# Optimization experiments

Measured on AMD Instinct MI355X. Metric: run time of the kernel, lower is better.

## Reference

```python
import jax, jax.numpy as jnp
import numpy as np

N, L, V = 8192, 50, 50000   # sentences, max words/sentence, vocab
D, H, O = 300, 150, 64      # embed dim, SAGE hidden, SAGE out
THRESH = 0.7
NEG = -1e9


def _sage_pool(h, A, mask, W1s, W1n, b1, W2s, W2n, b2, gw, gb):
    """Two-layer mean-aggregator SAGEConv + GlobalAttentionPooling, vectorized
    over N independent per-sentence graphs.
    h:[N,L,din] node feats, A:[N,L,L] bool adjacency (src u -> dst v), mask:[N,L] valid nodes."""
    Af = A.astype(h.dtype)
    deg = jnp.maximum(Af.sum(axis=1), 1.0)  # in-degree per dst node [N,L]

    def conv(x, Ws, Wn, b):
        m = jnp.einsum('nuv,nud->nvd', Af, x) / deg[..., None]  # mean of in-neighbors
        return x @ Ws + m @ Wn + b  # fc_self(x) + fc_neigh(mean)

    h1 = jax.nn.relu(conv(h, W1s, W1n, b1))
    h2 = conv(h1, W2s, W2n, b2)
    # global attention pooling: softmax(gate) over real nodes of each graph
    gate = jnp.squeeze(h2 @ gw, -1) + gb  # [N,L]
    attn = jax.nn.softmax(jnp.where(mask, gate, NEG), axis=-1)
    return jnp.einsum('nl,nld->nd', attn, h2)  # [N,O]


def setup_inputs() -> dict:
    key = jax.random.key(0)
    ks = jax.random.split(key, 32)
    pos = jnp.arange(L)
    lengths = jax.random.randint(ks[0], (N,), 5, L + 1)
    valid = pos[None, :] < lengths[:, None]  # [N,L] real-word mask (0 = pad)
    words = jax.random.randint(ks[1], (N, L), 1, V) * valid
    syntax_words = jax.random.randint(ks[2], (N, L), 1, V) * valid
    adj = jax.random.uniform(ks[3], (N, L, L)) < 0.08
    syntax_adj = (adj & valid[:, :, None] & valid[:, None, :]).astype(jnp.int32)
    hsg_feature = jax.random.normal(ks[4], (N, O), jnp.float32)

    def lin(k, i, o):
        return jax.random.normal(k, (i, o), jnp.float32) / np.sqrt(i)

    inp = {
        'words': words.astype(jnp.int32),
        'syntax_words': syntax_words.astype(jnp.int32),
        'syntax_adj': syntax_adj,
        'hsg_feature': hsg_feature,
        'embed': jax.random.normal(ks[5], (V, D), jnp.float32) * 0.1,
        'sem_W1s': lin(ks[6], D, H), 'sem_W1n': lin(ks[7], D, H), 'sem_b1': jnp.zeros((H,), jnp.float32),
        'sem_W2s': lin(ks[8], H, O), 'sem_W2n': lin(ks[9], H, O), 'sem_b2': jnp.zeros((O,), jnp.float32),
        'sem_gw': lin(ks[10], O, 1), 'sem_gb': jnp.zeros((1,), jnp.float32),
        'syn_W1s': lin(ks[11], D, H), 'syn_W1n': lin(ks[12], D, H), 'syn_b1': jnp.zeros((H,), jnp.float32),
        'syn_W2s': lin(ks[13], H, O), 'syn_W2n': lin(ks[14], H, O), 'syn_b2': jnp.zeros((O,), jnp.float32),
        'syn_gw': lin(ks[15], O, 1), 'syn_gb': jnp.zeros((1,), jnp.float32),
        'cls_w1': lin(ks[16], 3 * O, 128), 'cls_b1': jnp.zeros((128,), jnp.float32),
        'cls_w2': lin(ks[17], 128, 2), 'cls_b2': jnp.zeros((2,), jnp.float32),
    }
    return inp


def reference(words, syntax_words, syntax_adj, hsg_feature, embed,
              sem_W1s, sem_W1n, sem_b1, sem_W2s, sem_W2n, sem_b2, sem_gw, sem_gb,
              syn_W1s, syn_W1n, syn_b1, syn_W2s, syn_W2n, syn_b2, syn_gw, syn_gb,
              cls_w1, cls_b1, cls_w2, cls_b2):
    # --- semantic graph: per-sentence cosine-similarity thresholding ---
    mask = words > 0
    emb = embed[words]  # [N,L,D] gather
    nrm = emb / jnp.maximum(jnp.linalg.norm(emb, axis=-1, keepdims=True), 1e-8)
    cos = jnp.einsum('nld,nmd->nlm', nrm, nrm)  # [N,L,L]
    semA = (cos > THRESH) & mask[:, :, None] & mask[:, None, :]  # includes self-loops (cos=1)
    sem_feat = _sage_pool(emb, semA, mask,
                          sem_W1s, sem_W1n, sem_b1, sem_W2s, sem_W2n, sem_b2, sem_gw, sem_gb)
    # --- syntax graph: given per-sentence adjacency over its word ids ---
    syn_mask = syntax_words > 0
    syn_emb = embed[syntax_words]
    syn_feat = _sage_pool(syn_emb, syntax_adj.astype(bool), syn_mask,
                          syn_W1s, syn_W1n, syn_b1, syn_W2s, syn_W2n, syn_b2, syn_gw, syn_gb)
    # --- concat with HSG sentence state, classify ---
    feat = jnp.concatenate([sem_feat, syn_feat, hsg_feature], axis=-1)  # [N,192]
    hid = jax.nn.relu(feat @ cls_w1 + cls_b1)
    return hid @ cls_w2 + cls_b2  # [N,2]
```

## Files before the change

### kernel.cpp

```cpp
#include <hip/hip_runtime.h>

#define NS 8192
#define L  50

typedef unsigned short u16;
typedef unsigned int   u32;
typedef __attribute__((ext_vector_type(8))) __bf16 bf16x8;
typedef __attribute__((ext_vector_type(4))) float  f32x4;

#define OFF_X    0
#define OFF_TT   0
#define OFF_T2T  0
#define OFF_ATTN 0
#define OFF_H1   21760
#define OFF_RED  21760
#define OFF_M    43264
#define OFF_DIAG 43264
#define OFF_WID  52480
#define OFF_CLO  52736
#define OFF_CHI  52992
#define OFF_RDEG 53248
#define SMEM_SZ  53504

#define XSTR  328
#define TSTR  68
#define H1STR 168
#define MSTR  72

#define W1_ROWS 320
#define W1_KP   328
#define W2_ROWS 128
#define W2_KP   168

__device__ __forceinline__ u16 f2bf(float f) {
  u32 u = __float_as_uint(f);
  u += 0x7fffu + ((u >> 16) & 1u);
  return (u16)(u >> 16);
}
__device__ __forceinline__ float bf2f(u16 h) {
  return __uint_as_float(((u32)h) << 16);
}
__device__ __forceinline__ f32x4 mfma16(bf16x8 a, bf16x8 b, f32x4 c) {
  return __builtin_amdgcn_mfma_f32_16x16x32_bf16(a, b, c, 0, 0, 0);
}
__device__ __forceinline__ uint2 pack4bf(f32x4 c) {
  uint2 p;
  p.x = (u32)f2bf(c[0]) | ((u32)f2bf(c[1]) << 16);
  p.y = (u32)f2bf(c[2]) | ((u32)f2bf(c[3]) << 16);
  return p;
}
union BF8U { bf16x8 v; uint4 u; };
__device__ __forceinline__ bf16x8 ld_bf8_b64pair(const u16* p) {
  uint2 a = *(const uint2*)p;
  uint2 b = *(const uint2*)(p + 4);
  BF8U r; r.u = make_uint4(a.x, a.y, b.x, b.y);
  return r.v;
}

struct GParams {
  const int* words; const int* syn_words; const int* syn_adj;
  const float* embed;
  const float* sem_b1; const float* sem_b2; const float* sem_gw; const float* sem_gb;
  const float* syn_b1; const float* syn_b2; const float* syn_gw; const float* syn_gb;
  const u16* w1t_sem; const u16* w1t_syn; const u16* w2t_sem; const u16* w2t_syn;
  float* semf; float* synf;
};

__global__ __launch_bounds__(256, 3) void sage_kernel(GParams P) {
  __shared__ __align__(16) char smem[SMEM_SZ];
  int*   wid   = (int*)(smem + OFF_WID);
  u32*   clo   = (u32*)(smem + OFF_CLO);
  u32*   chi   = (u32*)(smem + OFF_CHI);
  float* rdegp = (float*)(smem + OFF_RDEG);
  float* diag  = (float*)(smem + OFF_DIAG);

  const int tid  = threadIdx.x;
  const int lane = tid & 63;
  const int w    = tid >> 6;
  const int ln   = lane & 15;
  const int quad = lane >> 4;

  const bool semg = (blockIdx.x < NS);
  const int  n    = semg ? blockIdx.x : (blockIdx.x - NS);

  const int*   wsrc = semg ? P.words   : P.syn_words;
  const u16*   W1T  = semg ? P.w1t_sem : P.w1t_syn;
  const u16*   W2T  = semg ? P.w2t_sem : P.w2t_syn;
  const float* b1g  = semg ? P.sem_b1  : P.syn_b1;
  const float* b2g  = semg ? P.sem_b2  : P.syn_b2;
  const float* gw   = semg ? P.sem_gw  : P.syn_gw;
  const float* gb   = semg ? P.sem_gb  : P.syn_gb;
  float* featout    = semg ? P.semf    : P.synf;

  const int jts[3] = {w, w + 4, 8 + (w & 1)};

  if (tid < 64) {
    wid[tid] = (tid < L) ? wsrc[(size_t)n * L + tid] : 0;
    clo[tid] = 0u; chi[tid] = 0u;
  }
  __syncthreads();

  for (int i = 0; i < 16; ++i) {
    const int v = w + 4 * i;
    const int word = wid[v];
    const float* src = P.embed + (size_t)word * 300;
    u16* xrow = (u16*)(smem + OFF_X) + v * XSTR;
    for (int l = lane; l < 82; l += 64) {
      uint2 pk = make_uint2(0u, 0u);
      if (word > 0 && l < 75) {
        float4 f = *(const float4*)(src + l * 4);
        pk.x = (u32)f2bf(f.x) | ((u32)f2bf(f.y) << 16);
        pk.y = (u32)f2bf(f.z) | ((u32)f2bf(f.w) << 16);
      }
      *(uint2*)(xrow + l * 4) = pk;
    }
  }
  __syncthreads();

  if (semg) {
    const f32x4 z4 = {0.f, 0.f, 0.f, 0.f};
    f32x4 g[4] = {z4, z4, z4, z4};
    const char* xb = smem + OFF_X;
    const int arow = (w * 16 + ln) * (XSTR * 2) + quad * 16;
    for (int kk = 0; kk < 10; ++kk) {
      bf16x8 a = *(const bf16x8*)(xb + arow + kk * 64);
      #pragma unroll
      for (int nt = 0; nt < 4; ++nt) {
        bf16x8 b = *(const bf16x8*)(xb + (nt * 16 + ln) * (XSTR * 2) + quad * 16 + kk * 64);
        g[nt] = mfma16(a, b, g[nt]);
      }
    }
    {
      const int r = ln - quad * 4;
      if (r >= 0 && r < 4) {
        #pragma unroll
        for (int nt = 0; nt < 4; ++nt) {
          if (nt == w) {
            float val = (r == 0) ? g[nt][0] : (r == 1) ? g[nt][1]
                      : (r == 2) ? g[nt][2] : g[nt][3];
            diag[w * 16 + ln] = val;
          }
        }
      }
    }
    __syncthreads();
    if (tid < 64) { float dd = diag[tid]; diag[tid] = 1.0f / sqrtf(fmaxf(dd, 1e-12f)); }
    __syncthreads();
    {
      const int ubase = w * 16 + quad * 4;
      float ru[4]; int uok[4];
      #pragma unroll
      for (int r = 0; r < 4; ++r) { ru[r] = diag[ubase + r]; uok[r] = wid[ubase + r] > 0; }
      #pragma unroll
      for (int nt = 0; nt < 4; ++nt) {
        const int v = nt * 16 + ln;
        const float rv = diag[v];
        const bool vok = wid[v] > 0;
        u32 nib = 0u;
        #pragma unroll
        for (int r = 0; r < 4; ++r) {
          float c = g[nt][r] * ru[r] * rv;
          if (vok && uok[r] && c > 0.7f) nib |= (1u << r);
        }
        if (nib) {
          if (ubase < 32) atomicOr(&clo[v], nib << ubase);
          else            atomicOr(&chi[v], nib << (ubase - 32));
        }
      }
    }
  } else {
    const int* abase = P.syn_adj + (size_t)n * (L * L);
    for (int v = w; v < L; v += 4) {
      int val = (lane < L) ? abase[lane * L + v] : 0;
      unsigned long long m = __ballot(val != 0);
      if (lane == 0) { clo[v] = (u32)m; chi[v] = (u32)(m >> 32); }
    }
  }
  __syncthreads();

  if (tid < 64) {
    int dg = __popc(clo[tid]) + __popc(chi[tid]);
    rdegp[tid] = 1.0f / (float)(dg > 0 ? dg : 1);
  }
  {
    const int v = lane, half = w;
    const u32 src = (half < 2) ? clo[v] : chi[v];
    const int sh = (half & 1) * 16;
    u16* Mrow = (u16*)(smem + OFF_M) + v * MSTR + half * 16;
    #pragma unroll
    for (int c = 0; c < 4; ++c) {
      uint2 pk;
      u32 b0 = (src >> (sh + 4 * c + 0)) & 1u;
      u32 b1 = (src >> (sh + 4 * c + 1)) & 1u;
      u32 b2 = (src >> (sh + 4 * c + 2)) & 1u;
      u32 b3 = (src >> (sh + 4 * c + 3)) & 1u;
      pk.x = (b0 ? 0x3F80u : 0u) | (b1 ? 0x3F800000u : 0u);
      pk.y = (b2 ? 0x3F80u : 0u) | (b3 ? 0x3F800000u : 0u);
      *(uint2*)(Mrow + 4 * c) = pk;
    }
  }

  const f32x4 z4 = {0.f, 0.f, 0.f, 0.f};
  f32x4 tacc[3][4], sacc[3][4];
  #pragma unroll
  for (int i = 0; i < 3; ++i)
    #pragma unroll
    for (int m = 0; m < 4; ++m) { tacc[i][m] = z4; sacc[i][m] = z4; }
  {
    const char* xb = smem + OFF_X;
    for (int kk = 0; kk < 10; ++kk) {
      bf16x8 x[4];
      #pragma unroll
      for (int m = 0; m < 4; ++m)
        x[m] = *(const bf16x8*)(xb + (m * 16 + ln) * (XSTR * 2) + quad * 16 + kk * 64);
      bf16x8 bn[3], as[3];
      #pragma unroll
      for (int i = 0; i < 3; ++i) {
        const int jt = jts[i];
        bn[i] = *(const bf16x8*)(W1T + (size_t)(jt * 16 + ln) * W1_KP + kk * 32 + quad * 8);
        as[i] = *(const bf16x8*)(W1T + (size_t)((jt + 10) * 16 + ln) * W1_KP + kk * 32 + quad * 8);
      }
      #pragma unroll
      for (int i = 0; i < 3; ++i)
        #pragma unroll
        for (int m = 0; m < 4; ++m) {
          tacc[i][m] = mfma16(x[m], bn[i], tacc[i][m]);
          sacc[i][m] = mfma16(as[i], x[m], sacc[i][m]);
        }
    }
  }
  __syncthreads();

  {
    u16* tt = (u16*)(smem + OFF_TT);
    #pragma unroll
    for (int i = 0; i < 3; ++i) {
      const int jt = jts[i];
      #pragma unroll
      for (int m = 0; m < 4; ++m) {
        const int v0 = m * 16 + quad * 4;
        *(uint2*)(tt + (jt * 16 + ln) * TSTR + v0) = pack4bf(tacc[i][m]);
      }
    }
  }

  bf16x8 mb0[4], mb1[4];
  {
    const u16* Mp = (const u16*)(smem + OFF_M);
    #pragma unroll
    for (int vt = 0; vt < 4; ++vt) {
      mb0[vt] = *(const bf16x8*)(Mp + (vt * 16 + ln) * MSTR + quad * 8);
      mb1[vt] = *(const bf16x8*)(Mp + (vt * 16 + ln) * MSTR + quad * 8 + 32);
    }
  }
  float rd[4];
  #pragma unroll
  for (int vt = 0; vt < 4; ++vt) rd[vt] = rdegp[vt * 16 + ln];
  {
    const u16* tt = (const u16*)(smem + OFF_TT);
    u16* h1p = (u16*)(smem + OFF_H1);
    #pragma unroll
    for (int i = 0; i < 3; ++i) {
      const int jt = jts[i];
      f32x4 gacc[4] = {z4, z4, z4, z4};
      const u16* tb = tt + (jt * 16 + ln) * TSTR + quad * 8;
      bf16x8 ta0 = ld_bf8_b64pair(tb);
      bf16x8 ta1 = ld_bf8_b64pair(tb + 32);
      #pragma unroll
      for (int vt = 0; vt < 4; ++vt) {
        gacc[vt] = mfma16(ta0, mb0[vt], gacc[vt]);
        gacc[vt] = mfma16(ta1, mb1[vt], gacc[vt]);
      }
      const int j0 = jt * 16 + quad * 4;
      float bv[4];
      #pragma unroll
      for (int r = 0; r < 4; ++r) { int j = j0 + r; bv[r] = (j < 150) ? b1g[j] : 0.f; }
      #pragma unroll
      for (int vt = 0; vt < 4; ++vt) {
        const int v = vt * 16 + ln;
        f32x4 hv;
        #pragma unroll
        for (int r = 0; r < 4; ++r)
          hv[r] = fmaxf(sacc[i][vt][r] + gacc[vt][r] * rd[vt] + bv[r], 0.f);
        *(uint2*)(h1p + v * H1STR + j0) = pack4bf(hv);
      }
    }
  }
  __syncthreads();

  f32x4 s2acc[4] = {z4, z4, z4, z4};
  f32x4 h2v[4];
  {
    f32x4 t2acc[4] = {z4, z4, z4, z4};
    const u16* h1p = (const u16*)(smem + OFF_H1);
    for (int kk = 0; kk < 5; ++kk) {
      bf16x8 h[4];
      #pragma unroll
      for (int t4 = 0; t4 < 4; ++t4)
        h[t4] = *(const bf16x8*)(h1p + (t4 * 16 + ln) * H1STR + kk * 32 + quad * 8);
      bf16x8 a2  = *(const bf16x8*)(W2T + (size_t)(w * 16 + ln) * W2_KP + kk * 32 + quad * 8);
      bf16x8 b2f = *(const bf16x8*)(W2T + (size_t)((4 + w) * 16 + ln) * W2_KP + kk * 32 + quad * 8);
      #pragma unroll
      for (int vt = 0; vt < 4; ++vt) {
        s2acc[vt] = mfma16(a2, h[vt], s2acc[vt]);
        t2acc[vt] = mfma16(h[vt], b2f, t2acc[vt]);
      }
    }
    u16* t2t = (u16*)(smem + OFF_T2T);
    #pragma unroll
    for (int m = 0; m < 4; ++m) {
      const int v0 = m * 16 + quad * 4;
      *(uint2*)(t2t + (w * 16 + ln) * TSTR + v0) = pack4bf(t2acc[m]);
    }
    f32x4 g2[4] = {z4, z4, z4, z4};
    const u16* t2b = t2t + (w * 16 + ln) * TSTR + quad * 8;
    bf16x8 u0 = ld_bf8_b64pair(t2b);
    bf16x8 u1 = ld_bf8_b64pair(t2b + 32);
    #pragma unroll
    for (int vt = 0; vt < 4; ++vt) {
      g2[vt] = mfma16(u0, mb0[vt], g2[vt]);
      g2[vt] = mfma16(u1, mb1[vt], g2[vt]);
    }
    const int j0q = w * 16 + quad * 4;
    float b2v[4];
    #pragma unroll
    for (int r = 0; r < 4; ++r) b2v[r] = b2g[j0q + r];
    #pragma unroll
    for (int vt = 0; vt < 4; ++vt)
      #pragma unroll
      for (int r = 0; r < 4; ++r)
        h2v[vt][r] = s2acc[vt][r] + g2[vt][r] * rd[vt] + b2v[r];
  }
  __syncthreads();

  {
    const int j0q = w * 16 + quad * 4;
    float gwv[4];
    #pragma unroll
    for (int r = 0; r < 4; ++r) gwv[r] = gw[j0q + r];
    float* redp = (float*)(smem + OFF_RED);
    #pragma unroll
    for (int vt = 0; vt < 4; ++vt) {
      float p = h2v[vt][0] * gwv[0] + h2v[vt][1] * gwv[1]
              + h2v[vt][2] * gwv[2] + h2v[vt][3] * gwv[3];
      redp[(vt * 16 + ln) * 17 + (w * 4 + quad)] = p;
    }
  }
  __syncthreads();

  if (tid < 64) {
    const float* redp = (const float*)(smem + OFF_RED);
    float g = gb[0];
    #pragma unroll
    for (int i = 0; i < 16; ++i) g += redp[tid * 17 + i];
    const bool val = wid[tid] > 0;
    g = val ? g : -1e30f;
    float mx = g;
    #pragma unroll
    for (int off = 32; off; off >>= 1) mx = fmaxf(mx, __shfl_xor(mx, off));
    float e = val ? __expf(g - mx) : 0.f;
    float ssum = e;
    #pragma unroll
    for (int off = 32; off; off >>= 1) ssum += __shfl_xor(ssum, off);
    ((float*)(smem + OFF_ATTN))[tid] = e / ssum;
  }
  __syncthreads();

  {
    const float* attnp = (const float*)(smem + OFF_ATTN);
    float av[4];
    #pragma unroll
    for (int vt = 0; vt < 4; ++vt) av[vt] = attnp[vt * 16 + ln];
    float xr[4];
    #pragma unroll
    for (int r = 0; r < 4; ++r) {
      float x = av[0] * h2v[0][r] + av[1] * h2v[1][r]
              + av[2] * h2v[2][r] + av[3] * h2v[3][r];
      #pragma unroll
      for (int off = 1; off < 16; off <<= 1) x += __shfl_xor(x, off);
      xr[r] = x;
    }
    if (ln == 0) {
      const int j0q = w * 16 + quad * 4;
      *(float4*)(featout + (size_t)n * 64 + j0q) = make_float4(xr[0], xr[1], xr[2], xr[3]);
    }
  }
}

__global__ void prep_w1(const float* Wn, const float* Ws, u16* dst) {
  int idx = blockIdx.x * 256 + threadIdx.x;
  if (idx >= W1_ROWS * W1_KP) return;
  int nn = idx / W1_KP, k = idx - nn * W1_KP;
  float v = 0.f;
  if (k < 300) {
    if (nn < 150) v = Wn[k * 150 + nn];
    else if (nn >= 160 && nn < 310) v = Ws[k * 150 + (nn - 160)];
  }
  dst[idx] = f2bf(v);
}
__global__ void prep_w2(const float* Ws, const float* Wn, u16* dst) {
  int idx = blockIdx.x * 256 + threadIdx.x;
  if (idx >= W2_ROWS * W2_KP) return;
  int nn = idx / W2_KP, k = idx - nn * W2_KP;
  float v = 0.f;
  if (k < 150) v = (nn < 64) ? Ws[k * 64 + nn] : Wn[k * 64 + (nn - 64)];
  dst[idx] = f2bf(v);
}

__global__ __launch_bounds__(128) void cls_kernel(const float* semf, const float* synf,
                                                  const float* hsg,
                                                  const float* w1, const float* b1,
                                                  const float* w2, const float* b2,
                                                  float* out) {
  __shared__ float feat[32][192];
  __shared__ float hid[32][132];
  const int r0 = blockIdx.x * 32;
  for (int idx = threadIdx.x; idx < 32 * 192; idx += 128) {
    int r = idx / 192, c = idx % 192;
    float v;
    if (c < 64)        v = semf[(size_t)(r0 + r) * 64 + c];
    else if (c < 128)  v = synf[(size_t)(r0 + r) * 64 + (c - 64)];
    else               v = hsg [(size_t)(r0 + r) * 64 + (c - 128)];
    feat[r][c] = v;
  }
  __syncthreads();
  {
    const int j = threadIdx.x;
    float acc[32];
    float bb = b1[j];
    #pragma unroll
    for (int r = 0; r < 32; ++r) acc[r] = bb;
    for (int k = 0; k < 192; ++k) {
      float ww = w1[(size_t)k * 128 + j];
      #pragma unroll
      for (int r = 0; r < 32; ++r) acc[r] += feat[r][k] * ww;
    }
    #pragma unroll
    for (int r = 0; r < 32; ++r) hid[r][j] = fmaxf(acc[r], 0.0f);
  }
  __syncthreads();
  if (threadIdx.x < 64) {
    const int r = threadIdx.x >> 1, o = threadIdx.x & 1;
    float a = b2[o];
    for (int h = 0; h < 128; ++h) a += hid[r][h] * w2[h * 2 + o];
    out[(size_t)(r0 + r) * 2 + o] = a;
  }
}

extern "C" void kernel_launch(void* const* d_in, const int* in_sizes, int n_in,
                              void* d_out, int out_size, void* d_ws, size_t ws_size,
                              hipStream_t stream) {
  GParams P;
  P.words     = (const int*)d_in[0];
  P.syn_words = (const int*)d_in[1];
  P.syn_adj   = (const int*)d_in[2];
  const float* hsg = (const float*)d_in[3];
  P.embed   = (const float*)d_in[4];
  const float* sem_W1s = (const float*)d_in[5];
  const float* sem_W1n = (const float*)d_in[6];
  P.sem_b1  = (const float*)d_in[7];
  const float* sem_W2s = (const float*)d_in[8];
  const float* sem_W2n = (const float*)d_in[9];
  P.sem_b2  = (const float*)d_in[10];
  P.sem_gw  = (const float*)d_in[11];
  P.sem_gb  = (const float*)d_in[12];
  const float* syn_W1s = (const float*)d_in[13];
  const float* syn_W1n = (const float*)d_in[14];
  P.syn_b1  = (const float*)d_in[15];
  const float* syn_W2s = (const float*)d_in[16];
  const float* syn_W2n = (const float*)d_in[17];
  P.syn_b2  = (const float*)d_in[18];
  P.syn_gw  = (const float*)d_in[19];
  P.syn_gb  = (const float*)d_in[20];
  const float* cls_w1 = (const float*)d_in[21];
  const float* cls_b1 = (const float*)d_in[22];
  const float* cls_w2 = (const float*)d_in[23];
  const float* cls_b2 = (const float*)d_in[24];

  float* semf = (float*)d_ws;
  float* synf = semf + (size_t)NS * 64;
  u16* w1t_sem = (u16*)((char*)d_ws + (size_t)4 * 1024 * 1024);
  u16* w1t_syn = w1t_sem + W1_ROWS * W1_KP;
  u16* w2t_sem = w1t_syn + W1_ROWS * W1_KP;
  u16* w2t_syn = w2t_sem + W2_ROWS * W2_KP;
  P.semf = semf; P.synf = synf;
  P.w1t_sem = w1t_sem; P.w1t_syn = w1t_syn;
  P.w2t_sem = w2t_sem; P.w2t_syn = w2t_syn;

  const int g1 = (W1_ROWS * W1_KP + 255) / 256;
  const int g2 = (W2_ROWS * W2_KP + 255) / 256;
  prep_w1<<<g1, 256, 0, stream>>>(sem_W1n, sem_W1s, w1t_sem);
  prep_w1<<<g1, 256, 0, stream>>>(syn_W1n, syn_W1s, w1t_syn);
  prep_w2<<<g2, 256, 0, stream>>>(sem_W2s, sem_W2n, w2t_sem);
  prep_w2<<<g2, 256, 0, stream>>>(syn_W2s, syn_W2n, w2t_syn);

  sage_kernel<<<2 * NS, 256, 0, stream>>>(P);
  cls_kernel<<<NS / 32, 128, 0, stream>>>(semf, synf, hsg, cls_w1, cls_b1,
                                          cls_w2, cls_b2, (float*)d_out);
}
```

Baseline: 882.9 us.

## Split layer-1 SAGE GEMM by role across warps and drop persistent adjacency fragments

Layer 1 is re-partitioned by role. Warps 0-1 compute the neighbour-transform tiles (5 each), which they write to LDS. Warps 2-3 compute the self-transform tiles and then do the adjacency aggregation and ReLU, replacing the earlier scheme where every warp did both for 3 tiles and tiles 8-9 were duplicated. Adjacency fragments are now reloaded from LDS at each use instead of being held in registers for the whole kernel, and accumulator count drops, to cut register pressure and redundant MFMA work. Embedding bf16 conversion becomes a cheaper round-half-up, and the LDS layout is repacked with a narrower M stride, at the cost of an extra barrier, load imbalance during aggregation, and possibly misaligned 16-byte LDS reads.

```diff
diff --git a/kernel.cpp b/kernel.cpp
--- a/kernel.cpp
+++ b/kernel.cpp
@@ -11,21 +11,21 @@
 #define OFF_X    0
 #define OFF_TT   0
 #define OFF_T2T  0
-#define OFF_ATTN 0
+#define OFF_RED  8704
+#define OFF_ATTN 13056
 #define OFF_H1   21760
-#define OFF_RED  21760
 #define OFF_M    43264
 #define OFF_DIAG 43264
-#define OFF_WID  52480
-#define OFF_CLO  52736
-#define OFF_CHI  52992
-#define OFF_RDEG 53248
-#define SMEM_SZ  53504
+#define OFF_WID  51968
+#define OFF_CLO  52224
+#define OFF_CHI  52480
+#define OFF_RDEG 52736
+#define SMEM_SZ  52992
 
 #define XSTR  328
 #define TSTR  68
 #define H1STR 168
-#define MSTR  72
+#define MSTR  68
 
 #define W1_ROWS 320
 #define W1_KP   328
@@ -36,9 +36,6 @@
   u32 u = __float_as_uint(f);
   u += 0x7fffu + ((u >> 16) & 1u);
   return (u16)(u >> 16);
-}
-__device__ __forceinline__ float bf2f(u16 h) {
-  return __uint_as_float(((u32)h) << 16);
 }
 __device__ __forceinline__ f32x4 mfma16(bf16x8 a, bf16x8 b, f32x4 c) {
   return __builtin_amdgcn_mfma_f32_16x16x32_bf16(a, b, c, 0, 0, 0);
@@ -91,8 +88,6 @@
   const float* gw   = semg ? P.sem_gw  : P.syn_gw;
   const float* gb   = semg ? P.sem_gb  : P.syn_gb;
   float* featout    = semg ? P.semf    : P.synf;
-
-  const int jts[3] = {w, w + 4, 8 + (w & 1)};
 
   if (tid < 64) {
     wid[tid] = (tid < L) ? wsrc[(size_t)n * L + tid] : 0;
@@ -109,16 +104,21 @@
       uint2 pk = make_uint2(0u, 0u);
       if (word > 0 && l < 75) {
         float4 f = *(const float4*)(src + l * 4);
-        pk.x = (u32)f2bf(f.x) | ((u32)f2bf(f.y) << 16);
-        pk.y = (u32)f2bf(f.z) | ((u32)f2bf(f.w) << 16);
+        u32 ax = __float_as_uint(f.x) + 0x8000u;
+        u32 ay = __float_as_uint(f.y) + 0x8000u;
+        u32 az = __float_as_uint(f.z) + 0x8000u;
+        u32 aw = __float_as_uint(f.w) + 0x8000u;
+        pk.x = (ax >> 16) | (ay & 0xffff0000u);
+        pk.y = (az >> 16) | (aw & 0xffff0000u);
       }
       *(uint2*)(xrow + l * 4) = pk;
     }
   }
   __syncthreads();
 
+  const f32x4 z4 = {0.f, 0.f, 0.f, 0.f};
+
   if (semg) {
-    const f32x4 z4 = {0.f, 0.f, 0.f, 0.f};
     f32x4 g[4] = {z4, z4, z4, z4};
     const char* xb = smem + OFF_X;
     const int arow = (w * 16 + ln) * (XSTR * 2) + quad * 16;
@@ -200,78 +200,86 @@
     }
   }
 
-  const f32x4 z4 = {0.f, 0.f, 0.f, 0.f};
-  f32x4 tacc[3][4], sacc[3][4];
+  f32x4 acc[5][4];
   #pragma unroll
-  for (int i = 0; i < 3; ++i)
-    #pragma unroll
-    for (int m = 0; m < 4; ++m) { tacc[i][m] = z4; sacc[i][m] = z4; }
+  for (int i = 0; i < 5; ++i)
+    #pragma unroll
+    for (int m = 0; m < 4; ++m) acc[i][m] = z4;
   {
     const char* xb = smem + OFF_X;
-    for (int kk = 0; kk < 10; ++kk) {
-      bf16x8 x[4];
-      #pragma unroll
-      for (int m = 0; m < 4; ++m)
-        x[m] = *(const bf16x8*)(xb + (m * 16 + ln) * (XSTR * 2) + quad * 16 + kk * 64);
-      bf16x8 bn[3], as[3];
-      #pragma unroll
-      for (int i = 0; i < 3; ++i) {
-        const int jt = jts[i];
-        bn[i] = *(const bf16x8*)(W1T + (size_t)(jt * 16 + ln) * W1_KP + kk * 32 + quad * 8);
-        as[i] = *(const bf16x8*)(W1T + (size_t)((jt + 10) * 16 + ln) * W1_KP + kk * 32 + quad * 8);
-      }
-      #pragma unroll
-      for (int i = 0; i < 3; ++i)
-        #pragma unroll
-        for (int m = 0; m < 4; ++m) {
-          tacc[i][m] = mfma16(x[m], bn[i], tacc[i][m]);
-          sacc[i][m] = mfma16(as[i], x[m], sacc[i][m]);
-        }
-    }
-  }
-  __syncthreads();
-
-  {
-    u16* tt = (u16*)(smem + OFF_TT);
-    #pragma unroll
-    for (int i = 0; i < 3; ++i) {
-      const int jt = jts[i];
-      #pragma unroll
-      for (int m = 0; m < 4; ++m) {
-        const int v0 = m * 16 + quad * 4;
-        *(uint2*)(tt + (jt * 16 + ln) * TSTR + v0) = pack4bf(tacc[i][m]);
-      }
-    }
-  }
-
-  bf16x8 mb0[4], mb1[4];
-  {
-    const u16* Mp = (const u16*)(smem + OFF_M);
-    #pragma unroll
-    for (int vt = 0; vt < 4; ++vt) {
-      mb0[vt] = *(const bf16x8*)(Mp + (vt * 16 + ln) * MSTR + quad * 8);
-      mb1[vt] = *(const bf16x8*)(Mp + (vt * 16 + ln) * MSTR + quad * 8 + 32);
-    }
-  }
+    if (w < 2) {
+      for (int kk = 0; kk < 10; ++kk) {
+        const int wo = kk * 32 + quad * 8;
+        bf16x8 x[4];
+        #pragma unroll
+        for (int m = 0; m < 4; ++m)
+          x[m] = *(const bf16x8*)(xb + (m * 16 + ln) * (XSTR * 2) + quad * 16 + kk * 64);
+        bf16x8 b[5];
+        #pragma unroll
+        for (int i = 0; i < 5; ++i)
+          b[i] = *(const bf16x8*)(W1T + (size_t)((w * 5 + i) * 16 + ln) * W1_KP + wo);
+        #pragma unroll
+        for (int i = 0; i < 5; ++i)
+          #pragma unroll
+          for (int m = 0; m < 4; ++m) acc[i][m] = mfma16(x[m], b[i], acc[i][m]);
+      }
+    } else {
+      for (int kk = 0; kk < 10; ++kk) {
+        const int wo = kk * 32 + quad * 8;
+        bf16x8 x[4];
+        #pragma unroll
+        for (int m = 0; m < 4; ++m)
+          x[m] = *(const bf16x8*)(xb + (m * 16 + ln) * (XSTR * 2) + quad * 16 + kk * 64);
+        bf16x8 b[5];
+        #pragma unroll
+        for (int i = 0; i < 5; ++i)
+          b[i] = *(const bf16x8*)(W1T + (size_t)((10 + (w - 2) * 5 + i) * 16 + ln) * W1_KP + wo);
+        #pragma unroll
+        for (int i = 0; i < 5; ++i)
+          #pragma unroll
+          for (int m = 0; m < 4; ++m) acc[i][m] = mfma16(b[i], x[m], acc[i][m]);
+      }
+    }
+  }
+  __syncthreads();
+
   float rd[4];
   #pragma unroll
   for (int vt = 0; vt < 4; ++vt) rd[vt] = rdegp[vt * 16 + ln];
-  {
+
+  if (w < 2) {
+    u16* tt = (u16*)(smem + OFF_TT);
+    #pragma unroll
+    for (int i = 0; i < 5; ++i) {
+      const int g = w * 5 + i;
+      #pragma unroll
+      for (int m = 0; m < 4; ++m) {
+        const int v0 = m * 16 + quad * 4;
+        *(uint2*)(tt + (g * 16 + ln) * TSTR + v0) = pack4bf(acc[i][m]);
+      }
+    }
+  }
+  __syncthreads();
+
+  if (w >= 2) {
     const u16* tt = (const u16*)(smem + OFF_TT);
+    const u16* Mp = (const u16*)(smem + OFF_M);
     u16* h1p = (u16*)(smem + OFF_H1);
     #pragma unroll
-    for (int i = 0; i < 3; ++i) {
-      const int jt = jts[i];
-      f32x4 gacc[4] = {z4, z4, z4, z4};
-      const u16* tb = tt + (jt * 16 + ln) * TSTR + quad * 8;
+    for (int i = 0; i < 5; ++i) {
+      const int g = (w - 2) * 5 + i;
+      const u16* tb = tt + (g * 16 + ln) * TSTR + quad * 8;
       bf16x8 ta0 = ld_bf8_b64pair(tb);
       bf16x8 ta1 = ld_bf8_b64pair(tb + 32);
+      f32x4 gacc[4] = {z4, z4, z4, z4};
       #pragma unroll
       for (int vt = 0; vt < 4; ++vt) {
-        gacc[vt] = mfma16(ta0, mb0[vt], gacc[vt]);
-        gacc[vt] = mfma16(ta1, mb1[vt], gacc[vt]);
-      }
-      const int j0 = jt * 16 + quad * 4;
+        bf16x8 m0 = *(const bf16x8*)(Mp + (vt * 16 + ln) * MSTR + quad * 8);
+        bf16x8 m1 = *(const bf16x8*)(Mp + (vt * 16 + ln) * MSTR + quad * 8 + 32);
+        gacc[vt] = mfma16(ta0, m0, gacc[vt]);
+        gacc[vt] = mfma16(ta1, m1, gacc[vt]);
+      }
+      const int j0 = g * 16 + quad * 4;
       float bv[4];
       #pragma unroll
       for (int r = 0; r < 4; ++r) { int j = j0 + r; bv[r] = (j < 150) ? b1g[j] : 0.f; }
@@ -281,25 +289,26 @@
         f32x4 hv;
         #pragma unroll
         for (int r = 0; r < 4; ++r)
-          hv[r] = fmaxf(sacc[i][vt][r] + gacc[vt][r] * rd[vt] + bv[r], 0.f);
+          hv[r] = fmaxf(acc[i][vt][r] + gacc[vt][r] * rd[vt] + bv[r], 0.f);
         *(uint2*)(h1p + v * H1STR + j0) = pack4bf(hv);
       }
     }
   }
   __syncthreads();
 
-  f32x4 s2acc[4] = {z4, z4, z4, z4};
   f32x4 h2v[4];
   {
+    f32x4 s2acc[4] = {z4, z4, z4, z4};
     f32x4 t2acc[4] = {z4, z4, z4, z4};
     const u16* h1p = (const u16*)(smem + OFF_H1);
     for (int kk = 0; kk < 5; ++kk) {
+      const int wo = kk * 32 + quad * 8;
       bf16x8 h[4];
       #pragma unroll
       for (int t4 = 0; t4 < 4; ++t4)
-        h[t4] = *(const bf16x8*)(h1p + (t4 * 16 + ln) * H1STR + kk * 32 + quad * 8);
-      bf16x8 a2  = *(const bf16x8*)(W2T + (size_t)(w * 16 + ln) * W2_KP + kk * 32 + quad * 8);
-      bf16x8 b2f = *(const bf16x8*)(W2T + (size_t)((4 + w) * 16 + ln) * W2_KP + kk * 32 + quad * 8);
+        h[t4] = *(const bf16x8*)(h1p + (t4 * 16 + ln) * H1STR + wo);
+      bf16x8 a2  = *(const bf16x8*)(W2T + (size_t)(w * 16 + ln) * W2_KP + wo);
+      bf16x8 b2f = *(const bf16x8*)(W2T + (size_t)((4 + w) * 16 + ln) * W2_KP + wo);
       #pragma unroll
       for (int vt = 0; vt < 4; ++vt) {
         s2acc[vt] = mfma16(a2, h[vt], s2acc[vt]);
@@ -312,14 +321,17 @@
       const int v0 = m * 16 + quad * 4;
       *(uint2*)(t2t + (w * 16 + ln) * TSTR + v0) = pack4bf(t2acc[m]);
     }
+    const u16* Mp = (const u16*)(smem + OFF_M);
     f32x4 g2[4] = {z4, z4, z4, z4};
     const u16* t2b = t2t + (w * 16 + ln) * TSTR + quad * 8;
     bf16x8 u0 = ld_bf8_b64pair(t2b);
     bf16x8 u1 = ld_bf8_b64pair(t2b + 32);
     #pragma unroll
     for (int vt = 0; vt < 4; ++vt) {
-      g2[vt] = mfma16(u0, mb0[vt], g2[vt]);
-      g2[vt] = mfma16(u1, mb1[vt], g2[vt]);
+      bf16x8 m0 = *(const bf16x8*)(Mp + (vt * 16 + ln) * MSTR + quad * 8);
+      bf16x8 m1 = *(const bf16x8*)(Mp + (vt * 16 + ln) * MSTR + quad * 8 + 32);
+      g2[vt] = mfma16(u0, m0, g2[vt]);
+      g2[vt] = mfma16(u1, m1, g2[vt]);
     }
     const int j0q = w * 16 + quad * 4;
     float b2v[4];
```

New measurement: 933.8 us. +5.8%, slower.
